# Optimization experiments

Measured on AMD Instinct MI355X. Metric: run time of the kernel, lower is better.

The kernel has to match this reference:

```python
import jax, jax.numpy as jnp
import numpy as np
from jax import lax

EPS = 1e-8
DIL = 4  # 2**(dilation-1) with dilation=3


def prelu(x, a):
    return jnp.where(x >= 0, x, a * x)


def cln(x):
    # cumulative layer norm over (channels, causal time window); gamma=1, beta=0
    # x: [B, M, L]
    M = x.shape[1]
    L = x.shape[2]
    cnt = (M * jnp.arange(1, L + 1, dtype=x.dtype))  # [L]
    csum = jnp.cumsum(jnp.sum(x, axis=1), axis=-1)           # [B, L]
    csq = jnp.cumsum(jnp.sum(x * x, axis=1), axis=-1)        # [B, L]
    mean = csum / cnt                                         # [B, L]
    var = csq / cnt - mean * mean                             # [B, L]
    return (x - mean[:, None, :]) / jnp.sqrt(var[:, None, :] + EPS)


def depthwise_conv(x, dw, db):
    # x: [B, H, L]; dw: [H, 1, P]; grouped conv, groups=H, 'same' padding, dilation DIL
    y = lax.conv_general_dilated(
        x, dw,
        window_strides=(1,),
        padding='SAME',
        rhs_dilation=(DIL,),
        dimension_numbers=('NCH', 'OIH', 'NCH'),
        feature_group_count=x.shape[1],
    )
    return y + db[None, :, None]


def setup_inputs() -> dict:
    key = jax.random.key(0)
    ks = jax.random.split(key, 9)
    Bc, H, P, Sc = 128, 512, 3, 128
    bsz, L = 4, 8000
    return {
        'x': jax.random.normal(ks[0], (bsz, Bc, L), dtype=jnp.float32),
        'W1': jax.random.normal(ks[1], (H, Bc), dtype=jnp.float32) * 0.05,
        'b1': jax.random.normal(ks[2], (H,), dtype=jnp.float32) * 0.02,
        'dw': jax.random.normal(ks[3], (H, 1, P), dtype=jnp.float32) * 0.1,
        'db': jax.random.normal(ks[4], (H,), dtype=jnp.float32) * 0.02,
        'Wout': jax.random.normal(ks[5], (Bc, H), dtype=jnp.float32) * 0.05,
        'bout': jax.random.normal(ks[6], (Bc,), dtype=jnp.float32) * 0.02,
        'Wskip': jax.random.normal(ks[7], (Sc, H), dtype=jnp.float32) * 0.05,
        'bskip': jax.random.normal(ks[8], (Sc,), dtype=jnp.float32) * 0.02,
        'a1': jnp.full((1,), 0.25, dtype=jnp.float32),
        'a2': jnp.full((1,), 0.25, dtype=jnp.float32),
    }


def reference(x, W1, b1, dw, db, Wout, bout, Wskip, bskip, a1, a2):
    res_x = x
    h = jnp.einsum('bcl,hc->bhl', x, W1) + b1[None, :, None]   # conv1x1 (k=1)
    h = prelu(h, a1)
    h = cln(h)
    h = depthwise_conv(h, dw, db)
    h = prelu(h, a2)
    h = cln(h)
    out = jnp.einsum('bhl,ch->bcl', h, Wout) + bout[None, :, None] + res_x
    skip = jnp.einsum('bhl,sh->bsl', h, Wskip) + bskip[None, :, None]
    return (out, skip)
```

## Files before the change

### kernel.cpp

```cpp
#include <hip/hip_runtime.h>

typedef unsigned short u16;
typedef unsigned int u32;
typedef __attribute__((ext_vector_type(8))) short bf16x8;
typedef __attribute__((ext_vector_type(4))) float f32x4;

#define Bn 4
#define Cn 128
#define Hn 512
#define Ln 8000
#define EPSf 1e-8f

__device__ __forceinline__ float bf2f(u32 v) { return __uint_as_float(v << 16); }
__device__ __forceinline__ u32 f2bf(float f) {
  u32 u = __float_as_uint(f);
  return (u + 0x7fffu + ((u >> 16) & 1u)) >> 16;
}
__device__ __forceinline__ void gl16(const void* g, void* l) {
  __builtin_amdgcn_global_load_lds((const __attribute__((address_space(1))) u32*)g,
                                   (__attribute__((address_space(3))) u32*)l, 16, 0, 0);
}

__global__ void k0_prep(const float* __restrict__ W1, const float* __restrict__ Wout,
                        const float* __restrict__ Wskip,
                        u16* __restrict__ W1b, u16* __restrict__ Wcatb,
                        float* __restrict__ Wsum)
{
  const int bid = blockIdx.x, tid = threadIdx.x;
  if (bid < 64) {
    const int base = (bid * 256 + tid) * 4;
#pragma unroll
    for (int t = 0; t < 4; ++t) {
      int i = base + t;
      int h = i >> 7, k = i & 127;
      int dbyte = h * 256 + (((k * 2) ^ ((h & 7) << 4)));
      W1b[dbyte >> 1] = (u16)f2bf(W1[h * Cn + k]);
    }
  } else if (bid < 192) {
    const int base = ((bid - 64) * 256 + tid) * 4;
#pragma unroll
    for (int t = 0; t < 4; ++t) {
      int j = base + t;
      int kt = j >> 14, r = j & 16383, c = r >> 6, kk = r & 63;
      int k = kt * 64 + kk;
      float v = (c < Cn) ? Wout[c * Hn + k] : Wskip[(c - Cn) * Hn + k];
      int dbyte = kt * 32768 + c * 128 + (((kk * 2) ^ ((c & 7) << 4)));
      Wcatb[dbyte >> 1] = (u16)f2bf(v);
    }
  } else {
    const int c = tid;
    const float* Wp = (c < Cn) ? (Wout + (size_t)c * Hn) : (Wskip + (size_t)(c - Cn) * Hn);
    float s = 0.f;
    for (int k = 0; k < Hn; ++k) s += Wp[k];
    Wsum[c] = s;
  }
}

__global__ __launch_bounds__(256, 2)
void k1_fused(const float* __restrict__ x, const u16* __restrict__ W1b,
              const float* __restrict__ b1, const float* __restrict__ a1p,
              u16* __restrict__ hT, float* __restrict__ sum1, float* __restrict__ sumsq1)
{
  __shared__ char regA[32768];
  __shared__ char xs[16384];
  __shared__ char stg[16384];
  __shared__ float b1s[512];
  const int bidx = blockIdx.x;
  const int b = bidx / 125, l0 = (bidx % 125) * 64;
  const int tid = threadIdx.x, ln = tid & 63, w = tid >> 6;
  const int ln15 = ln & 15, lq = ln >> 4;

  {
    const char* xb = (const char*)x + ((size_t)b * Cn * Ln + l0) * 4;
#pragma unroll
    for (int i = 0; i < 8; ++i) {
      int chunk = w * 8 + i;
      gl16(xb + (size_t)(chunk * 4 + (ln >> 4)) * (Ln * 4) + (ln & 15) * 16,
           regA + chunk * 1024);
    }
  }
  b1s[tid] = b1[tid];
  b1s[tid + 256] = b1[tid + 256];
  __syncthreads();
#pragma unroll
  for (int p = 0; p < 4; ++p) {
    int u = tid + p * 256;
    int l = u & 63, ui = u >> 6;
    u32 pk[4];
#pragma unroll
    for (int pp = 0; pp < 4; ++pp) {
      int c0 = ui * 8 + pp * 2;
      float f0 = *(const float*)(regA + c0 * 256 + l * 4);
      float f1 = *(const float*)(regA + (c0 + 1) * 256 + l * 4);
      pk[pp] = f2bf(f0) | (f2bf(f1) << 16);
    }
    uint4 st; st.x = pk[0]; st.y = pk[1]; st.z = pk[2]; st.w = pk[3];
    *(uint4*)(xs + l * 256 + ((ui * 16) ^ ((l & 7) << 4))) = st;
  }

  const float a1v = a1p[0];
  float sAcc = 0.f, qAcc = 0.f;

  for (int s = 0; s < 4; ++s) {
    __syncthreads();
#pragma unroll
    for (int i = 0; i < 8; ++i) {
      int chunk = w * 8 + i;
      gl16((const char*)W1b + s * 32768 + chunk * 1024 + ln * 16, regA + chunk * 1024);
    }
    __syncthreads();

    f32x4 acc[8];
    const f32x4 z4 = {0.f, 0.f, 0.f, 0.f};
#pragma unroll
    for (int rf = 0; rf < 8; ++rf) acc[rf] = z4;
#pragma unroll
    for (int kf = 0; kf < 4; ++kf) {
      const int brow = w * 16 + ln15;
      bf16x8 bfr = *(const bf16x8*)(xs + brow * 256 +
                                    ((kf * 64 + lq * 16) ^ ((brow & 7) << 4)));
#pragma unroll
      for (int rf = 0; rf < 8; ++rf) {
        int arow = rf * 16 + ln15;
        bf16x8 afr = *(const bf16x8*)(regA + arow * 256 +
                                      ((kf * 64 + lq * 16) ^ ((arow & 7) << 4)));
        acc[rf] = __builtin_amdgcn_mfma_f32_16x16x32_bf16(afr, bfr, acc[rf], 0, 0, 0);
      }
    }
#pragma unroll
    for (int rf = 0; rf < 8; ++rf) {
      int hb = s * 128 + rf * 16 + lq * 4;
      float v0 = acc[rf][0] + b1s[hb + 0]; v0 = v0 >= 0.f ? v0 : a1v * v0;
      float v1 = acc[rf][1] + b1s[hb + 1]; v1 = v1 >= 0.f ? v1 : a1v * v1;
      float v2 = acc[rf][2] + b1s[hb + 2]; v2 = v2 >= 0.f ? v2 : a1v * v2;
      float v3 = acc[rf][3] + b1s[hb + 3]; v3 = v3 >= 0.f ? v3 : a1v * v3;
      sAcc += v0 + v1 + v2 + v3;
      qAcc += v0 * v0 + v1 * v1 + v2 * v2 + v3 * v3;
      uint2 st2;
      st2.x = f2bf(v0) | (f2bf(v1) << 16);
      st2.y = f2bf(v2) | (f2bf(v3) << 16);
      *(uint2*)(stg + w * 4096 + ln15 * 256 +
                ((rf * 32 + lq * 8) ^ ((ln15 & 3) << 4))) = st2;
    }
#pragma unroll
    for (int p = 0; p < 4; ++p) {
      int lr = p * 4 + (ln >> 4);
      int j = ln & 15;
      uint4 v = *(const uint4*)(stg + w * 4096 + lr * 256 + ((j * 16) ^ ((lr & 3) << 4)));
      *(uint4*)((char*)hT + ((size_t)(b * Ln + l0 + w * 16 + lr)) * 1024 +
                s * 256 + j * 16) = v;
    }
  }
  sAcc += __shfl_xor(sAcc, 16); qAcc += __shfl_xor(qAcc, 16);
  sAcc += __shfl_xor(sAcc, 32); qAcc += __shfl_xor(qAcc, 32);
  if (lq == 0) {
    sum1[b * Ln + l0 + w * 16 + ln15] = sAcc;
    sumsq1[b * Ln + l0 + w * 16 + ln15] = qAcc;
  }
}

__global__ void k2_scan(const float* __restrict__ sum, const float* __restrict__ sumsq,
                        float* __restrict__ mean, float* __restrict__ rstd)
{
  const int b = blockIdx.x, tid = threadIdx.x;
  const int lane = tid & 63, w = tid >> 6;
  __shared__ float wts[4], wtq[4];
  float v[32], q[32];
  float ts = 0.f, tq = 0.f;
  const int base = tid * 32;
  const bool act = (tid < 250);
  if (act) {
#pragma unroll
    for (int i = 0; i < 8; ++i) {
      float4 a = *(const float4*)(sum + (size_t)b * Ln + base + i * 4);
      float4 c = *(const float4*)(sumsq + (size_t)b * Ln + base + i * 4);
      v[i * 4 + 0] = a.x; v[i * 4 + 1] = a.y; v[i * 4 + 2] = a.z; v[i * 4 + 3] = a.w;
      q[i * 4 + 0] = c.x; q[i * 4 + 1] = c.y; q[i * 4 + 2] = c.z; q[i * 4 + 3] = c.w;
    }
#pragma unroll
    for (int i = 0; i < 32; ++i) { ts += v[i]; tq += q[i]; }
  }
  float is = ts, iq = tq;
#pragma unroll
  for (int off = 1; off < 64; off <<= 1) {
    float a = __shfl_up(is, off);
    float c = __shfl_up(iq, off);
    if (lane >= off) { is += a; iq += c; }
  }
  float es = is - ts, eq = iq - tq;
  if (lane == 63) { wts[w] = is; wtq[w] = iq; }
  __syncthreads();
  for (int ww = 0; ww < w; ++ww) { es += wts[ww]; eq += wtq[ww]; }
  if (act) {
    float rs = es, rq = eq;
#pragma unroll
    for (int i = 0; i < 32; ++i) {
      rs += v[i]; rq += q[i];
      float cnt = 512.f * (float)(base + i + 1);
      float mn = rs / cnt;
      float var = fmaxf(rq / cnt - mn * mn, 0.f);
      v[i] = mn;
      q[i] = rsqrtf(var + EPSf);
    }
#pragma unroll
    for (int i = 0; i < 8; ++i) {
      float4 a; a.x = v[i*4+0]; a.y = v[i*4+1]; a.z = v[i*4+2]; a.w = v[i*4+3];
      float4 c; c.x = q[i*4+0]; c.y = q[i*4+1]; c.z = q[i*4+2]; c.w = q[i*4+3];
      *(float4*)(mean + (size_t)b * Ln + base + i * 4) = a;
      *(float4*)(rstd + (size_t)b * Ln + base + i * 4) = c;
    }
  }
}

__global__ __launch_bounds__(256, 2)
void k3_conv(const u16* __restrict__ hT, const float* __restrict__ mean1,
             const float* __restrict__ rstd1, const float* __restrict__ dw,
             const float* __restrict__ db, const float* __restrict__ a2p,
             u16* __restrict__ gT, float* __restrict__ sum2, float* __restrict__ sumsq2)
{
  __shared__ char hTs[73728];
  __shared__ float m1s[72], r1s[72];
  const int bidx = blockIdx.x;
  const int b = bidx / 125;
  const int l0 = (bidx % 125) * 64;
  const int tid = threadIdx.x;
  const int ln = tid & 63, w = tid >> 6;

  for (int i = 0; i < 18; ++i) {
    int chunk = w * 18 + i;
    int lr = l0 - 4 + chunk;
    int lc = lr < 0 ? 0 : (lr > Ln - 1 ? Ln - 1 : lr);
    gl16((const char*)hT + ((size_t)(b * Ln + lc)) * 1024 + ln * 16, hTs + chunk * 1024);
  }
  if (tid < 72) {
    int lr = l0 - 4 + tid;
    bool ok = (lr >= 0) && (lr < Ln);
    m1s[tid] = ok ? mean1[b * Ln + lr] : 0.f;
    r1s[tid] = ok ? rstd1[b * Ln + lr] : 0.f;
  }
  float d0[8], d1[8], d2[8], dbv[8];
#pragma unroll
  for (int e = 0; e < 8; ++e) {
    int hh = ln * 8 + e;
    d0[e] = dw[hh * 3 + 0]; d1[e] = dw[hh * 3 + 1]; d2[e] = dw[hh * 3 + 2];
    dbv[e] = db[hh];
  }
  const float a2v = a2p[0];
  __syncthreads();

  for (int it = 0; it < 16; ++it) {
    const int llo = w * 16 + it;
    const int l = l0 + llo;
    uint4 t0 = *reinterpret_cast<const uint4*>(hTs + (size_t)(llo) * 1024 + ln * 16);
    uint4 t1 = *reinterpret_cast<const uint4*>(hTs + (size_t)(llo + 4) * 1024 + ln * 16);
    uint4 t2 = *reinterpret_cast<const uint4*>(hTs + (size_t)(llo + 8) * 1024 + ln * 16);
    const float m0 = m1s[llo],     rr0 = r1s[llo];
    const float mC = m1s[llo + 4], rrC = r1s[llo + 4];
    const float m2v = m1s[llo + 8], rr2 = r1s[llo + 8];
    const u32* p0 = reinterpret_cast<const u32*>(&t0);
    const u32* p1 = reinterpret_cast<const u32*>(&t1);
    const u32* p2 = reinterpret_cast<const u32*>(&t2);
    float sv = 0.f, qv = 0.f;
    u32 outw[4];
#pragma unroll
    for (int pp = 0; pp < 4; ++pp) {
      float v01[2];
#pragma unroll
      for (int hi = 0; hi < 2; ++hi) {
        int e = pp * 2 + hi;
        u32 a0 = hi ? (p0[pp] >> 16) : (p0[pp] & 0xffffu);
        u32 a1b = hi ? (p1[pp] >> 16) : (p1[pp] & 0xffffu);
        u32 a2b = hi ? (p2[pp] >> 16) : (p2[pp] & 0xffffu);
        float nh0 = (bf2f(a0) - m0) * rr0;
        float nh1 = (bf2f(a1b) - mC) * rrC;
        float nh2 = (bf2f(a2b) - m2v) * rr2;
        float vv = fmaf(d0[e], nh0, fmaf(d1[e], nh1, fmaf(d2[e], nh2, dbv[e])));
        vv = vv >= 0.f ? vv : a2v * vv;
        sv += vv; qv += vv * vv;
        v01[hi] = vv;
      }
      outw[pp] = f2bf(v01[0]) | (f2bf(v01[1]) << 16);
    }
    uint4 st; st.x = outw[0]; st.y = outw[1]; st.z = outw[2]; st.w = outw[3];
    *reinterpret_cast<uint4*>((char*)gT + ((size_t)(b * Ln + l)) * 1024 +
                              (((ln * 16) ^ ((l & 7) << 4)))) = st;
#pragma unroll
    for (int off = 1; off < 64; off <<= 1) {
      sv += __shfl_xor(sv, off);
      qv += __shfl_xor(qv, off);
    }
    if (ln == 0) {
      sum2[b * Ln + l] = sv;
      sumsq2[b * Ln + l] = qv;
    }
  }
}

__global__ __launch_bounds__(256, 2)
void k5_gemm2(const u16* __restrict__ gT, const u16* __restrict__ Wcatb,
              const float* __restrict__ Wsum, const float* __restrict__ bout,
              const float* __restrict__ bskip, const float* __restrict__ mean2,
              const float* __restrict__ rstd2, const float* __restrict__ x,
              float* __restrict__ outp)
{
  __shared__ char Ab[2][32768];
  __shared__ char Bb[2][8192];
  const int bidx = blockIdx.x;
  const int b = bidx / 125;
  const int l0 = (bidx % 125) * 64;
  const int tid = threadIdx.x;
  const int ln = tid & 63, w = tid >> 6;
  const int ln15 = ln & 15, lq = ln >> 4;

  auto stage = [&](int kt, int bi) {
    const char* Asrc = (const char*)Wcatb + kt * 32768;
#pragma unroll
    for (int i = 0; i < 8; ++i) {
      int chunk = w * 8 + i;
      gl16(Asrc + chunk * 1024 + ln * 16, Ab[bi] + chunk * 1024);
    }
#pragma unroll
    for (int j = 0; j < 2; ++j) {
      int chunk = w * 2 + j;
      int lrow = chunk * 8 + (ln >> 3);
      int pos = (ln & 7) * 16;
      gl16((const char*)gT + ((size_t)(b * Ln + l0 + lrow)) * 1024 + kt * 128 + pos,
           Bb[bi] + chunk * 1024);
    }
  };

  f32x4 acc[4][4];
  const f32x4 z4 = {0.f, 0.f, 0.f, 0.f};
#pragma unroll
  for (int i = 0; i < 4; ++i)
#pragma unroll
    for (int j = 0; j < 4; ++j) acc[i][j] = z4;

  const int c0w = w * 64;
  stage(0, 0);
  __syncthreads();
  for (int kt = 0; kt < 8; ++kt) {
    const int cur = kt & 1;
    if (kt < 7) stage(kt + 1, cur ^ 1);
    const char* Ac = Ab[cur];
    const char* Bc = Bb[cur];
#pragma unroll
    for (int ks = 0; ks < 2; ++ks) {
      bf16x8 bfr[4];
#pragma unroll
      for (int cf = 0; cf < 4; ++cf) {
        int brow = cf * 16 + ln15;
        int off = ((ks * 64 + lq * 16) ^ ((brow & 7) << 4));
        bfr[cf] = *reinterpret_cast<const bf16x8*>(Bc + brow * 128 + off);
      }
#pragma unroll
      for (int rf = 0; rf < 4; ++rf) {
        int arow = c0w + rf * 16 + ln15;
        int aoff = ((ks * 64 + lq * 16) ^ ((arow & 7) << 4));
        bf16x8 afr = *reinterpret_cast<const bf16x8*>(Ac + arow * 128 + aoff);
#pragma unroll
        for (int cf = 0; cf < 4; ++cf)
          acc[rf][cf] = __builtin_amdgcn_mfma_f32_16x16x32_bf16(afr, bfr[cf], acc[rf][cf], 0, 0, 0);
      }
    }
    __syncthreads();
  }

  float wsr[4][4], bir[4][4];
#pragma unroll
  for (int rf = 0; rf < 4; ++rf)
#pragma unroll
    for (int r = 0; r < 4; ++r) {
      int c = c0w + rf * 16 + lq * 4 + r;
      wsr[rf][r] = Wsum[c];
      bir[rf][r] = (c < Cn) ? bout[c] : bskip[c - Cn];
    }
  char* stg = &Ab[0][0];
#pragma unroll
  for (int cf = 0; cf < 4; ++cf) {
    const int ll = cf * 16 + ln15;
    const int l = l0 + ll;
    const float m2 = mean2[b * Ln + l];
    const float r2 = rstd2[b * Ln + l];
#pragma unroll
    for (int rf = 0; rf < 4; ++rf) {
#pragma unroll
      for (int r = 0; r < 4; ++r) {
        int c = c0w + rf * 16 + lq * 4 + r;
        float o = r2 * (acc[rf][cf][r] - m2 * wsr[rf][r]) + bir[rf][r];
        *(float*)(stg + c * 256 + ((((ll >> 2) * 16) ^ ((c & 7) << 4)) + (ll & 3) * 4)) = o;
      }
    }
  }
  __syncthreads();
  const size_t OUTOFF = (size_t)Bn * Cn * Ln;
#pragma unroll
  for (int p = 0; p < 16; ++p) {
    int i = p * 256 + tid;
    int c = i >> 4, j = i & 15;
    float4 v = *(const float4*)(stg + c * 256 + ((j * 16) ^ ((c & 7) << 4)));
    if (c < Cn) {
      float4 xv = *(const float4*)(x + ((size_t)(b * Cn + c)) * Ln + l0 + j * 4);
      v.x += xv.x; v.y += xv.y; v.z += xv.z; v.w += xv.w;
      *(float4*)(outp + ((size_t)(b * Cn + c)) * Ln + l0 + j * 4) = v;
    } else {
      *(float4*)(outp + OUTOFF + ((size_t)(b * Cn + c - Cn)) * Ln + l0 + j * 4) = v;
    }
  }
}

extern "C" void kernel_launch(void* const* d_in, const int* in_sizes, int n_in,
                              void* d_out, int out_size, void* d_ws, size_t ws_size,
                              hipStream_t stream)
{
  const float* x     = (const float*)d_in[0];
  const float* W1    = (const float*)d_in[1];
  const float* b1    = (const float*)d_in[2];
  const float* dw    = (const float*)d_in[3];
  const float* db    = (const float*)d_in[4];
  const float* Wout  = (const float*)d_in[5];
  const float* bout  = (const float*)d_in[6];
  const float* Wskip = (const float*)d_in[7];
  const float* bskip = (const float*)d_in[8];
  const float* a1    = (const float*)d_in[9];
  const float* a2    = (const float*)d_in[10];
  float* outp = (float*)d_out;

  char* ws = (char*)d_ws;
  u16* hT     = (u16*)(ws);
  u16* gT     = (u16*)(ws + 32768000);
  u16* W1b    = (u16*)(ws + 65536000);
  u16* Wcatb  = (u16*)(ws + 65667072);
  float* Wsum   = (float*)(ws + 65929216);
  float* sum1   = (float*)(ws + 65930240);
  float* sumsq1 = (float*)(ws + 66058240);
  float* mean1  = (float*)(ws + 66186240);
  float* rstd1  = (float*)(ws + 66314240);
  float* sum2   = (float*)(ws + 66442240);
  float* sumsq2 = (float*)(ws + 66570240);
  float* mean2  = (float*)(ws + 66698240);
  float* rstd2  = (float*)(ws + 66826240);
  (void)in_sizes; (void)n_in; (void)out_size; (void)ws_size;

  hipLaunchKernelGGL(k0_prep, dim3(193), dim3(256), 0, stream,
                     W1, Wout, Wskip, W1b, Wcatb, Wsum);
  hipLaunchKernelGGL(k1_fused, dim3(Bn * 125), dim3(256), 0, stream,
                     x, W1b, b1, a1, hT, sum1, sumsq1);
  hipLaunchKernelGGL(k2_scan, dim3(Bn), dim3(256), 0, stream,
                     sum1, sumsq1, mean1, rstd1);
  hipLaunchKernelGGL(k3_conv, dim3(Bn * 125), dim3(256), 0, stream,
                     hT, mean1, rstd1, dw, db, a2, gT, sum2, sumsq2);
  hipLaunchKernelGGL(k2_scan, dim3(Bn), dim3(256), 0, stream,
                     sum2, sumsq2, mean2, rstd2);
  hipLaunchKernelGGL(k5_gemm2, dim3(Bn * 125), dim3(256), 0, stream,
                     gT, Wcatb, Wsum, bout, bskip, mean2, rstd2, x, outp);
}
```

Baseline: 90.41 us.

## Recompute depthwise conv inside final GEMM instead of materializing gT

The conv kernel now only computes the per-time sums for the second cumulative norm and no longer writes the bf16 conv output gT. The final GEMM kernel recomputes the depthwise conv, norm and PReLU per K-tile from hT in shared memory, then feeds the result to the MFMAs. hT gets a new XOR swizzle so the restaged rows avoid LDS bank conflicts. This removes a 32 MB write and read of gT, but the conv is now done twice and the GEMM loses its A/B double buffering, adding more syncs per K step.

```diff
diff --git a/kernel.cpp b/kernel.cpp
--- a/kernel.cpp
+++ b/kernel.cpp
@@ -20,6 +20,7 @@
   __builtin_amdgcn_global_load_lds((const __attribute__((address_space(1))) u32*)g,
                                    (__attribute__((address_space(3))) u32*)l, 16, 0, 0);
 }
+
 
 __global__ void k0_prep(const float* __restrict__ W1, const float* __restrict__ Wout,
                         const float* __restrict__ Wskip,
@@ -147,8 +148,9 @@
       int lr = p * 4 + (ln >> 4);
       int j = ln & 15;
       uint4 v = *(const uint4*)(stg + w * 4096 + lr * 256 + ((j * 16) ^ ((lr & 3) << 4)));
+      int jp = (j & 8) | ((j & 7) ^ ((lr + 4) & 7));
       *(uint4*)((char*)hT + ((size_t)(b * Ln + l0 + w * 16 + lr)) * 1024 +
-                s * 256 + j * 16) = v;
+                s * 256 + jp * 16) = v;
     }
   }
   sAcc += __shfl_xor(sAcc, 16); qAcc += __shfl_xor(qAcc, 16);
@@ -213,10 +215,10 @@
 }
 
 __global__ __launch_bounds__(256, 2)
-void k3_conv(const u16* __restrict__ hT, const float* __restrict__ mean1,
+void k3_sums(const u16* __restrict__ hT, const float* __restrict__ mean1,
              const float* __restrict__ rstd1, const float* __restrict__ dw,
              const float* __restrict__ db, const float* __restrict__ a2p,
-             u16* __restrict__ gT, float* __restrict__ sum2, float* __restrict__ sumsq2)
+             float* __restrict__ sum2, float* __restrict__ sumsq2)
 {
   __shared__ char hTs[73728];
   __shared__ float m1s[72], r1s[72];
@@ -248,12 +250,13 @@
   const float a2v = a2p[0];
   __syncthreads();
 
+  const int gB = (ln & 56) << 4;
   for (int it = 0; it < 16; ++it) {
     const int llo = w * 16 + it;
     const int l = l0 + llo;
-    uint4 t0 = *reinterpret_cast<const uint4*>(hTs + (size_t)(llo) * 1024 + ln * 16);
-    uint4 t1 = *reinterpret_cast<const uint4*>(hTs + (size_t)(llo + 4) * 1024 + ln * 16);
-    uint4 t2 = *reinterpret_cast<const uint4*>(hTs + (size_t)(llo + 8) * 1024 + ln * 16);
+    uint4 t0 = *(const uint4*)(hTs + (size_t)(llo) * 1024 + gB + (((ln ^ llo) & 7) << 4));
+    uint4 t1 = *(const uint4*)(hTs + (size_t)(llo + 4) * 1024 + gB + (((ln ^ (llo + 4)) & 7) << 4));
+    uint4 t2 = *(const uint4*)(hTs + (size_t)(llo + 8) * 1024 + gB + (((ln ^ llo) & 7) << 4));
     const float m0 = m1s[llo],     rr0 = r1s[llo];
     const float mC = m1s[llo + 4], rrC = r1s[llo + 4];
     const float m2v = m1s[llo + 8], rr2 = r1s[llo + 8];
@@ -261,10 +264,8 @@
     const u32* p1 = reinterpret_cast<const u32*>(&t1);
     const u32* p2 = reinterpret_cast<const u32*>(&t2);
     float sv = 0.f, qv = 0.f;
-    u32 outw[4];
 #pragma unroll
     for (int pp = 0; pp < 4; ++pp) {
-      float v01[2];
 #pragma unroll
       for (int hi = 0; hi < 2; ++hi) {
         int e = pp * 2 + hi;
@@ -277,13 +278,8 @@
         float vv = fmaf(d0[e], nh0, fmaf(d1[e], nh1, fmaf(d2[e], nh2, dbv[e])));
         vv = vv >= 0.f ? vv : a2v * vv;
         sv += vv; qv += vv * vv;
-        v01[hi] = vv;
-      }
-      outw[pp] = f2bf(v01[0]) | (f2bf(v01[1]) << 16);
-    }
-    uint4 st; st.x = outw[0]; st.y = outw[1]; st.z = outw[2]; st.w = outw[3];
-    *reinterpret_cast<uint4*>((char*)gT + ((size_t)(b * Ln + l)) * 1024 +
-                              (((ln * 16) ^ ((l & 7) << 4)))) = st;
+      }
+    }
 #pragma unroll
     for (int off = 1; off < 64; off <<= 1) {
       sv += __shfl_xor(sv, off);
@@ -297,14 +293,21 @@
 }
 
 __global__ __launch_bounds__(256, 2)
-void k5_gemm2(const u16* __restrict__ gT, const u16* __restrict__ Wcatb,
+void k5_fused(const u16* __restrict__ hT, const u16* __restrict__ Wcatb,
               const float* __restrict__ Wsum, const float* __restrict__ bout,
-              const float* __restrict__ bskip, const float* __restrict__ mean2,
-              const float* __restrict__ rstd2, const float* __restrict__ x,
-              float* __restrict__ outp)
+              const float* __restrict__ bskip,
+              const float* __restrict__ mean1, const float* __restrict__ rstd1,
+              const float* __restrict__ mean2, const float* __restrict__ rstd2,
+              const float* __restrict__ dw, const float* __restrict__ db,
+              const float* __restrict__ a2p,
+              const float* __restrict__ x, float* __restrict__ outp)
 {
-  __shared__ char Ab[2][32768];
-  __shared__ char Bb[2][8192];
+  __shared__ char Ab[32768];
+  __shared__ char Hb[9216];
+  __shared__ char Gb[8192];
+  __shared__ float dwdb[2048];
+  __shared__ float m1s[72], r1s[72];
+
   const int bidx = blockIdx.x;
   const int b = bidx / 125;
   const int l0 = (bidx % 125) * 64;
@@ -312,22 +315,45 @@
   const int ln = tid & 63, w = tid >> 6;
   const int ln15 = ln & 15, lq = ln >> 4;
 
-  auto stage = [&](int kt, int bi) {
+  auto stageH = [&](int kt) {
+    for (int ch = w; ch < 9; ch += 4) {
+      int row = ch * 8 + (ln >> 3);
+      int lr = l0 - 4 + row;
+      int lc = lr < 0 ? 0 : (lr > Ln - 1 ? Ln - 1 : lr);
+      gl16((const char*)hT + ((size_t)(b * Ln + lc)) * 1024 + kt * 128 + (ln & 7) * 16,
+           Hb + ch * 1024);
+    }
+  };
+  auto stageA = [&](int kt) {
     const char* Asrc = (const char*)Wcatb + kt * 32768;
 #pragma unroll
     for (int i = 0; i < 8; ++i) {
       int chunk = w * 8 + i;
-      gl16(Asrc + chunk * 1024 + ln * 16, Ab[bi] + chunk * 1024);
-    }
-#pragma unroll
-    for (int j = 0; j < 2; ++j) {
-      int chunk = w * 2 + j;
-      int lrow = chunk * 8 + (ln >> 3);
-      int pos = (ln & 7) * 16;
-      gl16((const char*)gT + ((size_t)(b * Ln + l0 + lrow)) * 1024 + kt * 128 + pos,
-           Bb[bi] + chunk * 1024);
+      gl16(Asrc + chunk * 1024 + ln * 16, Ab + chunk * 1024);
     }
   };
+
+  stageA(0);
+  stageH(0);
+  if (tid < 72) {
+    int lr = l0 - 4 + tid;
+    bool ok = (lr >= 0) && (lr < Ln);
+    m1s[tid] = ok ? mean1[b * Ln + lr] : 0.f;
+    r1s[tid] = ok ? rstd1[b * Ln + lr] : 0.f;
+  }
+  {
+    int h2 = tid * 2;
+    dwdb[h2 * 4 + 0] = dw[h2 * 3 + 0];
+    dwdb[h2 * 4 + 1] = dw[h2 * 3 + 1];
+    dwdb[h2 * 4 + 2] = dw[h2 * 3 + 2];
+    dwdb[h2 * 4 + 3] = db[h2];
+    dwdb[h2 * 4 + 4] = dw[h2 * 3 + 3];
+    dwdb[h2 * 4 + 5] = dw[h2 * 3 + 4];
+    dwdb[h2 * 4 + 6] = dw[h2 * 3 + 5];
+    dwdb[h2 * 4 + 7] = db[h2 + 1];
+  }
+  const float a2v = a2p[0];
+  __syncthreads();
 
   f32x4 acc[4][4];
   const f32x4 z4 = {0.f, 0.f, 0.f, 0.f};
@@ -335,15 +361,49 @@
   for (int i = 0; i < 4; ++i)
 #pragma unroll
     for (int j = 0; j < 4; ++j) acc[i][j] = z4;
-
   const int c0w = w * 64;
-  stage(0, 0);
-  __syncthreads();
+
   for (int kt = 0; kt < 8; ++kt) {
-    const int cur = kt & 1;
-    if (kt < 7) stage(kt + 1, cur ^ 1);
-    const char* Ac = Ab[cur];
-    const char* Bc = Bb[cur];
+    {
+      const int r0 = ln, r1 = ln + 4, r2 = ln + 8;
+      const float m0 = m1s[r0], q0 = r1s[r0];
+      const float mA = m1s[r1], qA = r1s[r1];
+      const float mB = m1s[r2], qB = r1s[r2];
+      const int kk0 = r0 & 7, kk1 = r1 & 7;
+#pragma unroll
+      for (int uu = 0; uu < 2; ++uu) {
+        const int grp = w + uu * 4;
+        uint4 t0 = *(const uint4*)(Hb + r0 * 128 + ((grp ^ kk0) << 4));
+        uint4 t1 = *(const uint4*)(Hb + r1 * 128 + ((grp ^ kk1) << 4));
+        uint4 t2 = *(const uint4*)(Hb + r2 * 128 + ((grp ^ kk0) << 4));
+        const u32* p0 = (const u32*)&t0;
+        const u32* p1 = (const u32*)&t1;
+        const u32* p2 = (const u32*)&t2;
+        u32 ow[4];
+#pragma unroll
+        for (int pp = 0; pp < 4; ++pp) {
+          float vv[2];
+#pragma unroll
+          for (int hi = 0; hi < 2; ++hi) {
+            const int e = pp * 2 + hi;
+            float4 dv = *(const float4*)(&dwdb[(kt * 64 + grp * 8 + e) * 4]);
+            u32 a0 = hi ? (p0[pp] >> 16) : (p0[pp] & 0xffffu);
+            u32 a1 = hi ? (p1[pp] >> 16) : (p1[pp] & 0xffffu);
+            u32 a2b = hi ? (p2[pp] >> 16) : (p2[pp] & 0xffffu);
+            float nh0 = (bf2f(a0) - m0) * q0;
+            float nh1 = (bf2f(a1) - mA) * qA;
+            float nh2 = (bf2f(a2b) - mB) * qB;
+            float v = fmaf(dv.x, nh0, fmaf(dv.y, nh1, fmaf(dv.z, nh2, dv.w)));
+            vv[hi] = v >= 0.f ? v : a2v * v;
+          }
+          ow[pp] = f2bf(vv[0]) | (f2bf(vv[1]) << 16);
+        }
+        uint4 st; st.x = ow[0]; st.y = ow[1]; st.z = ow[2]; st.w = ow[3];
+        *(uint4*)(Gb + ln * 128 + ((grp ^ (ln & 7)) << 4)) = st;
+      }
+    }
+    __syncthreads();
+    if (kt < 7) stageH(kt + 1);
 #pragma unroll
     for (int ks = 0; ks < 2; ++ks) {
       bf16x8 bfr[4];
@@ -351,19 +411,20 @@
       for (int cf = 0; cf < 4; ++cf) {
         int brow = cf * 16 + ln15;
         int off = ((ks * 64 + lq * 16) ^ ((brow & 7) << 4));
-        bfr[cf] = *reinterpret_cast<const bf16x8*>(Bc + brow * 128 + off);
+        bfr[cf] = *(const bf16x8*)(Gb + brow * 128 + off);
       }
 #pragma unroll
       for (int rf = 0; rf < 4; ++rf) {
         int arow = c0w + rf * 16 + ln15;
         int aoff = ((ks * 64 + lq * 16) ^ ((arow & 7) << 4));
-        bf16x8 afr = *reinterpret_cast<const bf16x8*>(Ac + arow * 128 + aoff);
+        bf16x8 afr = *(const bf16x8*)(Ab + arow * 128 + aoff);
 #pragma unroll
         for (int cf = 0; cf < 4; ++cf)
           acc[rf][cf] = __builtin_amdgcn_mfma_f32_16x16x32_bf16(afr, bfr[cf], acc[rf][cf], 0, 0, 0);
       }
     }
     __syncthreads();
+    if (kt < 7) stageA(kt + 1);
   }
 
   float wsr[4][4], bir[4][4];
@@ -375,36 +436,42 @@
       wsr[rf][r] = Wsum[c];
       bir[rf][r] = (c < Cn) ? bout[c] : bskip[c - Cn];
     }
-  char* stg = &Ab[0][0];
-#pragma unroll
-  for (int cf = 0; cf < 4; ++cf) {
-    const int ll = cf * 16 + ln15;
-    const int l = l0 + ll;
-    const float m2 = mean2[b * Ln + l];
-    const float r2 = rstd2[b * Ln + l];
-#pragma unroll
-    for (int rf = 0; rf < 4; ++rf) {
-#pragma unroll
-      for (int r = 0; r < 4; ++r) {
-        int c = c0w + rf * 16 + lq * 4 + r;
-        float o = r2 * (acc[rf][cf][r] - m2 * wsr[rf][r]) + bir[rf][r];
-        *(float*)(stg + c * 256 + ((((ll >> 2) * 16) ^ ((c & 7) << 4)) + (ll & 3) * 4)) = o;
-      }
-    }
-  }
-  __syncthreads();
   const size_t OUTOFF = (size_t)Bn * Cn * Ln;
-#pragma unroll
-  for (int p = 0; p < 16; ++p) {
-    int i = p * 256 + tid;
-    int c = i >> 4, j = i & 15;
-    float4 v = *(const float4*)(stg + c * 256 + ((j * 16) ^ ((c & 7) << 4)));
-    if (c < Cn) {
-      float4 xv = *(const float4*)(x + ((size_t)(b * Cn + c)) * Ln + l0 + j * 4);
-      v.x += xv.x; v.y += xv.y; v.z += xv.z; v.w += xv.w;
-      *(float4*)(outp + ((size_t)(b * Cn + c)) * Ln + l0 + j * 4) = v;
-    } else {
-      *(float4*)(outp + OUTOFF + ((size_t)(b * Cn + c - Cn)) * Ln + l0 + j * 4) = v;
+  char* stg = Ab;
+#pragma unroll
+  for (int p = 0; p < 2; ++p) {
+    if (p) __syncthreads();
+#pragma unroll
+    for (int cc = 0; cc < 2; ++cc) {
+      const int cf = p * 2 + cc;
+      const int ll = cc * 16 + ln15;
+      const int l = l0 + cf * 16 + ln15;
+      const float m2 = mean2[b * Ln + l];
+      const float r2 = rstd2[b * Ln + l];
+#pragma unroll
+      for (int rf = 0; rf < 4; ++rf) {
+#pragma unroll
+        for (int r = 0; r < 4; ++r) {
+          int c = c0w + rf * 16 + lq * 4 + r;
+          float o = r2 * (acc[rf][cf][r] - m2 * wsr[rf][r]) + bir[rf][r];
+          *(float*)(stg + c * 128 + ((((ll >> 2) ^ (c & 7)) << 4)) + (ll & 3) * 4) = o;
+        }
+      }
+    }
+    __syncthreads();
+#pragma unroll
+    for (int pp = 0; pp < 8; ++pp) {
+      int i = pp * 256 + tid;
+      int c = i >> 3, j = i & 7;
+      float4 v = *(const float4*)(stg + c * 128 + (((j ^ (c & 7)) << 4)));
+      int lcol = l0 + p * 32 + j * 4;
+      if (c < Cn) {
+        float4 xv = *(const float4*)(x + ((size_t)(b * Cn + c)) * Ln + lcol);
+        v.x += xv.x; v.y += xv.y; v.z += xv.z; v.w += xv.w;
+        *(float4*)(outp + ((size_t)(b * Cn + c)) * Ln + lcol) = v;
+      } else {
+        *(float4*)(outp + OUTOFF + ((size_t)(b * Cn + c - Cn)) * Ln + lcol) = v;
+      }
     }
   }
 }
@@ -428,7 +495,6 @@
 
   char* ws = (char*)d_ws;
   u16* hT     = (u16*)(ws);
-  u16* gT     = (u16*)(ws + 32768000);
   u16* W1b    = (u16*)(ws + 65536000);
   u16* Wcatb  = (u16*)(ws + 65667072);
   float* Wsum   = (float*)(ws + 65929216);
@@ -448,10 +514,11 @@
                      x, W1b, b1, a1, hT, sum1, sumsq1);
   hipLaunchKernelGGL(k2_scan, dim3(Bn), dim3(256), 0, stream,
                      sum1, sumsq1, mean1, rstd1);
-  hipLaunchKernelGGL(k3_conv, dim3(Bn * 125), dim3(256), 0, stream,
-                     hT, mean1, rstd1, dw, db, a2, gT, sum2, sumsq2);
+  hipLaunchKernelGGL(k3_sums, dim3(Bn * 125), dim3(256), 0, stream,
+                     hT, mean1, rstd1, dw, db, a2, sum2, sumsq2);
   hipLaunchKernelGGL(k2_scan, dim3(Bn), dim3(256), 0, stream,
                      sum2, sumsq2, mean2, rstd2);
-  hipLaunchKernelGGL(k5_gemm2, dim3(Bn * 125), dim3(256), 0, stream,
-                     gT, Wcatb, Wsum, bout, bskip, mean2, rstd2, x, outp);
-}
+  hipLaunchKernelGGL(k5_fused, dim3(Bn * 125), dim3(256), 0, stream,
+                     hT, Wcatb, Wsum, bout, bskip, mean1, rstd1, mean2, rstd2,
+                     dw, db, a2, x, outp);
+}
```

New measurement: 96.08 us (median of 2 runs). 6.3% more time.

## Shrink LDS footprint in three kernels to fit three blocks per CU

Applied to the files above, without the earlier changes.

The k1 kernel reuses the weight tile buffer as its output staging area instead of keeping a separate staging array, which adds an extra barrier. The k3 conv kernel halves its time tile to 32 columns and launches twice as many blocks, which cuts its shared halo buffer. The k5 GEMM drops double-buffering of the weight tile, loading it synchronously after each k-step, and writes its output epilogue in two halves through a smaller staging area. All three kernels raise launch bounds to 3 blocks per CU, trading pipelining and halo reuse for occupancy.

```diff
diff --git a/kernel.cpp b/kernel.cpp
--- a/kernel.cpp
+++ b/kernel.cpp
@@ -56,14 +56,13 @@
   }
 }
 
-__global__ __launch_bounds__(256, 2)
+__global__ __launch_bounds__(256, 3)
 void k1_fused(const float* __restrict__ x, const u16* __restrict__ W1b,
               const float* __restrict__ b1, const float* __restrict__ a1p,
               u16* __restrict__ hT, float* __restrict__ sum1, float* __restrict__ sumsq1)
 {
   __shared__ char regA[32768];
   __shared__ char xs[16384];
-  __shared__ char stg[16384];
   __shared__ float b1s[512];
   const int bidx = blockIdx.x;
   const int b = bidx / 125, l0 = (bidx % 125) * 64;
@@ -100,6 +99,7 @@
 
   const float a1v = a1p[0];
   float sAcc = 0.f, qAcc = 0.f;
+  char* stg = regA;
 
   for (int s = 0; s < 4; ++s) {
     __syncthreads();
@@ -127,6 +127,8 @@
         acc[rf] = __builtin_amdgcn_mfma_f32_16x16x32_bf16(afr, bfr, acc[rf], 0, 0, 0);
       }
     }
+    __syncthreads();
+
 #pragma unroll
     for (int rf = 0; rf < 8; ++rf) {
       int hb = s * 128 + rf * 16 + lq * 4;
@@ -212,27 +214,27 @@
   }
 }
 
-__global__ __launch_bounds__(256, 2)
+__global__ __launch_bounds__(256, 3)
 void k3_conv(const u16* __restrict__ hT, const float* __restrict__ mean1,
              const float* __restrict__ rstd1, const float* __restrict__ dw,
              const float* __restrict__ db, const float* __restrict__ a2p,
              u16* __restrict__ gT, float* __restrict__ sum2, float* __restrict__ sumsq2)
 {
-  __shared__ char hTs[73728];
-  __shared__ float m1s[72], r1s[72];
+  __shared__ char hTs[40960];
+  __shared__ float m1s[40], r1s[40];
   const int bidx = blockIdx.x;
-  const int b = bidx / 125;
-  const int l0 = (bidx % 125) * 64;
+  const int b = bidx / 250;
+  const int l0 = (bidx % 250) * 32;
   const int tid = threadIdx.x;
   const int ln = tid & 63, w = tid >> 6;
 
-  for (int i = 0; i < 18; ++i) {
-    int chunk = w * 18 + i;
+  for (int i = 0; i < 10; ++i) {
+    int chunk = w * 10 + i;
     int lr = l0 - 4 + chunk;
     int lc = lr < 0 ? 0 : (lr > Ln - 1 ? Ln - 1 : lr);
     gl16((const char*)hT + ((size_t)(b * Ln + lc)) * 1024 + ln * 16, hTs + chunk * 1024);
   }
-  if (tid < 72) {
+  if (tid < 40) {
     int lr = l0 - 4 + tid;
     bool ok = (lr >= 0) && (lr < Ln);
     m1s[tid] = ok ? mean1[b * Ln + lr] : 0.f;
@@ -248,8 +250,8 @@
   const float a2v = a2p[0];
   __syncthreads();
 
-  for (int it = 0; it < 16; ++it) {
-    const int llo = w * 16 + it;
+  for (int it = 0; it < 8; ++it) {
+    const int llo = w * 8 + it;
     const int l = l0 + llo;
     uint4 t0 = *reinterpret_cast<const uint4*>(hTs + (size_t)(llo) * 1024 + ln * 16);
     uint4 t1 = *reinterpret_cast<const uint4*>(hTs + (size_t)(llo + 4) * 1024 + ln * 16);
@@ -296,14 +298,14 @@
   }
 }
 
-__global__ __launch_bounds__(256, 2)
+__global__ __launch_bounds__(256, 3)
 void k5_gemm2(const u16* __restrict__ gT, const u16* __restrict__ Wcatb,
               const float* __restrict__ Wsum, const float* __restrict__ bout,
               const float* __restrict__ bskip, const float* __restrict__ mean2,
               const float* __restrict__ rstd2, const float* __restrict__ x,
               float* __restrict__ outp)
 {
-  __shared__ char Ab[2][32768];
+  __shared__ char Ab[32768];
   __shared__ char Bb[2][8192];
   const int bidx = blockIdx.x;
   const int b = bidx / 125;
@@ -312,13 +314,15 @@
   const int ln = tid & 63, w = tid >> 6;
   const int ln15 = ln & 15, lq = ln >> 4;
 
-  auto stage = [&](int kt, int bi) {
+  auto stageA = [&](int kt) {
     const char* Asrc = (const char*)Wcatb + kt * 32768;
 #pragma unroll
     for (int i = 0; i < 8; ++i) {
       int chunk = w * 8 + i;
-      gl16(Asrc + chunk * 1024 + ln * 16, Ab[bi] + chunk * 1024);
-    }
+      gl16(Asrc + chunk * 1024 + ln * 16, Ab + chunk * 1024);
+    }
+  };
+  auto stageB = [&](int kt, int bi) {
 #pragma unroll
     for (int j = 0; j < 2; ++j) {
       int chunk = w * 2 + j;
@@ -337,13 +341,12 @@
     for (int j = 0; j < 4; ++j) acc[i][j] = z4;
 
   const int c0w = w * 64;
-  stage(0, 0);
+  stageA(0);
+  stageB(0, 0);
   __syncthreads();
   for (int kt = 0; kt < 8; ++kt) {
     const int cur = kt & 1;
-    if (kt < 7) stage(kt + 1, cur ^ 1);
-    const char* Ac = Ab[cur];
-    const char* Bc = Bb[cur];
+    if (kt < 7) stageB(kt + 1, cur ^ 1);
 #pragma unroll
     for (int ks = 0; ks < 2; ++ks) {
       bf16x8 bfr[4];
@@ -351,19 +354,23 @@
       for (int cf = 0; cf < 4; ++cf) {
         int brow = cf * 16 + ln15;
         int off = ((ks * 64 + lq * 16) ^ ((brow & 7) << 4));
-        bfr[cf] = *reinterpret_cast<const bf16x8*>(Bc + brow * 128 + off);
+        bfr[cf] = *reinterpret_cast<const bf16x8*>(Bb[cur] + brow * 128 + off);
       }
 #pragma unroll
       for (int rf = 0; rf < 4; ++rf) {
         int arow = c0w + rf * 16 + ln15;
         int aoff = ((ks * 64 + lq * 16) ^ ((arow & 7) << 4));
-        bf16x8 afr = *reinterpret_cast<const bf16x8*>(Ac + arow * 128 + aoff);
+        bf16x8 afr = *reinterpret_cast<const bf16x8*>(Ab + arow * 128 + aoff);
 #pragma unroll
         for (int cf = 0; cf < 4; ++cf)
           acc[rf][cf] = __builtin_amdgcn_mfma_f32_16x16x32_bf16(afr, bfr[cf], acc[rf][cf], 0, 0, 0);
       }
     }
     __syncthreads();
+    if (kt < 7) {
+      stageA(kt + 1);
+      __syncthreads();
+    }
   }
 
   float wsr[4][4], bir[4][4];
@@ -375,36 +382,42 @@
       wsr[rf][r] = Wsum[c];
       bir[rf][r] = (c < Cn) ? bout[c] : bskip[c - Cn];
     }
-  char* stg = &Ab[0][0];
-#pragma unroll
-  for (int cf = 0; cf < 4; ++cf) {
-    const int ll = cf * 16 + ln15;
-    const int l = l0 + ll;
-    const float m2 = mean2[b * Ln + l];
-    const float r2 = rstd2[b * Ln + l];
-#pragma unroll
-    for (int rf = 0; rf < 4; ++rf) {
-#pragma unroll
-      for (int r = 0; r < 4; ++r) {
-        int c = c0w + rf * 16 + lq * 4 + r;
-        float o = r2 * (acc[rf][cf][r] - m2 * wsr[rf][r]) + bir[rf][r];
-        *(float*)(stg + c * 256 + ((((ll >> 2) * 16) ^ ((c & 7) << 4)) + (ll & 3) * 4)) = o;
-      }
-    }
-  }
-  __syncthreads();
   const size_t OUTOFF = (size_t)Bn * Cn * Ln;
-#pragma unroll
-  for (int p = 0; p < 16; ++p) {
-    int i = p * 256 + tid;
-    int c = i >> 4, j = i & 15;
-    float4 v = *(const float4*)(stg + c * 256 + ((j * 16) ^ ((c & 7) << 4)));
-    if (c < Cn) {
-      float4 xv = *(const float4*)(x + ((size_t)(b * Cn + c)) * Ln + l0 + j * 4);
-      v.x += xv.x; v.y += xv.y; v.z += xv.z; v.w += xv.w;
-      *(float4*)(outp + ((size_t)(b * Cn + c)) * Ln + l0 + j * 4) = v;
-    } else {
-      *(float4*)(outp + OUTOFF + ((size_t)(b * Cn + c - Cn)) * Ln + l0 + j * 4) = v;
+  char* stg = Ab;
+#pragma unroll
+  for (int p = 0; p < 2; ++p) {
+    if (p) __syncthreads();
+#pragma unroll
+    for (int cc = 0; cc < 2; ++cc) {
+      const int cf = p * 2 + cc;
+      const int ll = cc * 16 + ln15;
+      const int l = l0 + cf * 16 + ln15;
+      const float m2 = mean2[b * Ln + l];
+      const float r2 = rstd2[b * Ln + l];
+#pragma unroll
+      for (int rf = 0; rf < 4; ++rf) {
+#pragma unroll
+        for (int r = 0; r < 4; ++r) {
+          int c = c0w + rf * 16 + lq * 4 + r;
+          float o = r2 * (acc[rf][cf][r] - m2 * wsr[rf][r]) + bir[rf][r];
+          *(float*)(stg + c * 128 + ((((ll >> 2) ^ (c & 7)) << 4)) + (ll & 3) * 4) = o;
+        }
+      }
+    }
+    __syncthreads();
+#pragma unroll
+    for (int pp = 0; pp < 8; ++pp) {
+      int i = pp * 256 + tid;
+      int c = i >> 3, j = i & 7;
+      float4 v = *(const float4*)(stg + c * 128 + (((j ^ (c & 7)) << 4)));
+      int lcol = l0 + p * 32 + j * 4;
+      if (c < Cn) {
+        float4 xv = *(const float4*)(x + ((size_t)(b * Cn + c)) * Ln + lcol);
+        v.x += xv.x; v.y += xv.y; v.z += xv.z; v.w += xv.w;
+        *(float4*)(outp + ((size_t)(b * Cn + c)) * Ln + lcol) = v;
+      } else {
+        *(float4*)(outp + OUTOFF + ((size_t)(b * Cn + c - Cn)) * Ln + lcol) = v;
+      }
     }
   }
 }
@@ -448,7 +461,7 @@
                      x, W1b, b1, a1, hT, sum1, sumsq1);
   hipLaunchKernelGGL(k2_scan, dim3(Bn), dim3(256), 0, stream,
                      sum1, sumsq1, mean1, rstd1);
-  hipLaunchKernelGGL(k3_conv, dim3(Bn * 125), dim3(256), 0, stream,
+  hipLaunchKernelGGL(k3_conv, dim3(Bn * 250), dim3(256), 0, stream,
                      hT, mean1, rstd1, dw, db, a2, gT, sum2, sumsq2);
   hipLaunchKernelGGL(k2_scan, dim3(Bn), dim3(256), 0, stream,
                      sum2, sumsq2, mean2, rstd2);
```

After: 92.48 us. 1.02x slower.
